# Performance work log

Hardware: AMD Instinct MI355X
Metric: run time of the kernel (lower is better)

## Reference

```python
import jax, jax.numpy as jnp
import numpy as np

B, S, H, HKV, D, BS = 2, 2048, 32, 8, 128, 16
HIDDEN = H * D            # 4096
G = H // HKV              # 4 query heads per kv head
NB = S // BS              # 128 blocks per sequence
SCALE = D ** -0.5


def setup_inputs() -> dict:
    key = jax.random.key(0)
    k1, k2, k3 = jax.random.split(key, 3)
    T = B * S
    hidden_states = jax.random.normal(k1, (T, HIDDEN), dtype=jnp.float32)
    w_qkv = jax.random.normal(k2, (HIDDEN, HIDDEN + 2 * HKV * D), dtype=jnp.float32) * 0.02
    w_out = jax.random.normal(k3, (HIDDEN, HIDDEN), dtype=jnp.float32) * 0.02
    k_cache = jnp.zeros((B * NB, HKV, BS, D), dtype=jnp.float32)
    v_cache = jnp.zeros((B * NB, HKV, BS, D), dtype=jnp.float32)
    block_tables = jnp.arange(B * NB, dtype=jnp.int32).reshape(B, NB)
    return {"hidden_states": hidden_states, "w_qkv": w_qkv, "w_out": w_out,
            "k_cache": k_cache, "v_cache": v_cache, "block_tables": block_tables}


def reference(hidden_states, w_qkv, w_out, k_cache, v_cache, block_tables):
    # qkv projection on packed tokens [T, hidden]
    qkv = hidden_states @ w_qkv
    q, k, v = jnp.split(qkv, [HIDDEN, HIDDEN + HKV * D], axis=-1)
    q = q.reshape(B, S, H, D)
    k = k.reshape(B, S, HKV, D)
    v = v.reshape(B, S, HKV, D)

    # --- paged KV store: scatter per-block pages into cache via block_tables ---
    # [B, NB, BS, HKV, D] -> page layout [B, NB, HKV, BS, D]
    k_pages = k.reshape(B, NB, BS, HKV, D).transpose(0, 1, 3, 2, 4)
    v_pages = v.reshape(B, NB, BS, HKV, D).transpose(0, 1, 3, 2, 4)
    k_cache = k_cache.at[block_tables].set(k_pages)
    v_cache = v_cache.at[block_tables].set(v_pages)

    # --- paged KV gather for prefill attention ---
    kg = k_cache[block_tables].transpose(0, 2, 1, 3, 4).reshape(B, HKV, S, D)
    vg = v_cache[block_tables].transpose(0, 2, 1, 3, 4).reshape(B, HKV, S, D)

    # GQA causal attention: group query heads per kv head
    qh = q.transpose(0, 2, 1, 3).reshape(B, HKV, G, S, D)
    scores = jnp.einsum('bhgqd,bhkd->bhgqk', qh, kg) * SCALE
    causal = jnp.tril(jnp.ones((S, S), dtype=bool))
    scores = jnp.where(causal, scores, -jnp.inf)
    attn = jax.nn.softmax(scores, axis=-1)
    out = jnp.einsum('bhgqk,bhkd->bhgqd', attn, vg)   # [B,HKV,G,S,D]
    out = out.reshape(B, H, S, D).transpose(0, 2, 1, 3).reshape(B * S, HIDDEN)
    return out @ w_out
```

## Files before the change

kernel.cpp:

```cpp
#include <hip/hip_runtime.h>

#define BB 2
#define SS 2048
#define HH 32
#define HKV 8
#define DD 128
#define HIDDEN 4096
#define NQK 6144
#define TT 4096
#define SCALE 0.08838834764831843f
#define SCALE_LOG2E 0.12751743444f

typedef __attribute__((ext_vector_type(8), __may_alias__)) short short8;
typedef __attribute__((ext_vector_type(4), __may_alias__)) short short4v;
typedef __attribute__((ext_vector_type(4), __may_alias__)) float floatx4;

__device__ __forceinline__ short f2bf(float x) {
    unsigned u = __builtin_bit_cast(unsigned, x);
    u += 0x7FFFu + ((u >> 16) & 1u);
    return (short)(u >> 16);
}

__device__ __forceinline__ void gload_lds16(const short* g, short* l) {
    __builtin_amdgcn_global_load_lds((const __attribute__((address_space(1))) void*)g,
                                     (__attribute__((address_space(3))) void*)l, 16, 0, 0);
}

__global__ __launch_bounds__(256) void cvt_f32_bf16(const float* __restrict__ src,
                                                    short* __restrict__ dst) {
    int i = blockIdx.x * 256 + threadIdx.x;
    typedef __attribute__((ext_vector_type(4), __may_alias__)) float f4;
    f4 v = ((const f4*)src)[i];
    short4v o = { f2bf(v.x), f2bf(v.y), f2bf(v.z), f2bf(v.w) };
    ((short4v*)dst)[i] = o;
}

__global__ __launch_bounds__(256) void transpose_cvt(const float* __restrict__ src,
                                                     short* __restrict__ dst,
                                                     int rows, int cols) {
    __shared__ float t[32][33];
    int tx = threadIdx.x, ty = threadIdx.y;
    int c0 = blockIdx.x * 32, r0 = blockIdx.y * 32;
#pragma unroll
    for (int i = 0; i < 32; i += 8) t[ty + i][tx] = src[(size_t)(r0 + ty + i) * cols + c0 + tx];
    __syncthreads();
#pragma unroll
    for (int i = 0; i < 32; i += 8)
        dst[(size_t)(c0 + ty + i) * rows + r0 + tx] = f2bf(t[tx][ty + i]);
}

__global__ __launch_bounds__(256) void build_vt(const short* __restrict__ qkv,
                                                short* __restrict__ vt) {
    __shared__ short t[32][33];
    int tx = threadIdx.x, ty = threadIdx.y;
    int s0 = blockIdx.x * 32, d0 = blockIdx.y * 32;
    int bh = blockIdx.z; int b = bh >> 3, hk = bh & 7;
#pragma unroll
    for (int i = 0; i < 32; i += 8)
        t[ty + i][tx] = qkv[(size_t)(b * SS + s0 + ty + i) * NQK + 5120 + hk * DD + d0 + tx];
    __syncthreads();
#pragma unroll
    for (int i = 0; i < 32; i += 8)
        vt[(size_t)(bh * DD + d0 + ty + i) * SS + s0 + tx] = t[tx][ty + i];
}

template <int OUT_BF16>
__global__ __launch_bounds__(512, 2) void gemm_bt(const short* __restrict__ A,
                                                  const short* __restrict__ Bt,
                                                  void* __restrict__ Cout,
                                                  int M, int N, int K) {
    (void)M;
    __shared__ __align__(16) short smem[65536];
    const int tid  = threadIdx.x;
    const int wave = tid >> 6, lane = tid & 63;
    const int qn = lane & 15, quad = lane >> 4;
    const int wm = wave >> 2, wn = wave & 3;

    int nwg = gridDim.x * gridDim.y;
    int bid = blockIdx.y * gridDim.x + blockIdx.x;
    int q8 = nwg >> 3, r8 = nwg & 7, xcd = bid & 7, boff = bid >> 3;
    int swz = (xcd < r8 ? xcd * (q8 + 1) : r8 * (q8 + 1) + (xcd - r8) * q8) + boff;
    const int n0 = (swz % gridDim.x) * 256;
    const int m0 = (swz / gridDim.x) * 256;

    const int NT = K >> 6;

    const int srow = tid >> 3;
    const int scg  = (tid & 7) ^ (srow & 7);
    const short* aS = A  + (size_t)(m0 + srow) * K + scg * 8;
    const short* bS = Bt + (size_t)(n0 + srow) * K + scg * 8;
    const int lwo = wave * 512;

#define STAGE_A(buf, blk, tt) gload_lds16(aS + (size_t)(blk) * 64 * K + (size_t)(tt) * 64, \
                                          smem + (buf) + (blk) * 4096 + lwo)
#define STAGE_B(buf, blk, tt) gload_lds16(bS + (size_t)(blk) * 64 * K + (size_t)(tt) * 64, \
                                          smem + (buf) + 16384 + (blk) * 4096 + lwo)

    const int xorm  = (qn & 7) << 3;
    const int a_row = (wm * 128 + qn) * 64;
    const int b_row = (wn * 64 + qn) * 64;
    const int col0  = (quad * 8) ^ xorm;
    const int col1  = col0 ^ 32;

#pragma unroll
    for (int blk = 0; blk < 4; blk++) { STAGE_A(0, blk, 0); STAGE_B(0, blk, 0); }
    if (NT > 1) {
#pragma unroll
        for (int blk = 0; blk < 4; blk++) { STAGE_A(32768, blk, 1); STAGE_B(32768, blk, 1); }
        asm volatile("s_waitcnt vmcnt(8)" ::: "memory");
    } else {
        asm volatile("s_waitcnt vmcnt(0)" ::: "memory");
    }
    __builtin_amdgcn_s_barrier();

    floatx4 acc[8][4] = {};

#pragma unroll 2
    for (int t = 0; t < NT; ++t) {
        const int cb = (t & 1) << 15;
        const short* Ab = smem + cb;
        const short* Bb = smem + cb + 16384;
        short8 a[4][2], b0[2][2], b1[2][2], a2[4][2];

#pragma unroll
        for (int mt = 0; mt < 4; mt++) {
            a[mt][0] = *(const short8*)(Ab + a_row + mt * 1024 + col0);
            a[mt][1] = *(const short8*)(Ab + a_row + mt * 1024 + col1);
        }
#pragma unroll
        for (int nt = 0; nt < 2; nt++) {
            b0[nt][0] = *(const short8*)(Bb + b_row + nt * 1024 + col0);
            b0[nt][1] = *(const short8*)(Bb + b_row + nt * 1024 + col1);
        }
        asm volatile("s_waitcnt lgkmcnt(8)" ::: "memory");
        __builtin_amdgcn_s_barrier();
        asm volatile("s_waitcnt lgkmcnt(0)" ::: "memory");
        __builtin_amdgcn_s_setprio(1);
#pragma unroll
        for (int mt = 0; mt < 4; mt++)
#pragma unroll
            for (int nt = 0; nt < 2; nt++) {
                acc[mt][nt] = __builtin_amdgcn_mfma_f32_16x16x32_bf16(a[mt][0], b0[nt][0], acc[mt][nt], 0, 0, 0);
                acc[mt][nt] = __builtin_amdgcn_mfma_f32_16x16x32_bf16(a[mt][1], b0[nt][1], acc[mt][nt], 0, 0, 0);
            }
        __builtin_amdgcn_s_setprio(0);
        __builtin_amdgcn_s_barrier();

#pragma unroll
        for (int nt = 0; nt < 2; nt++) {
            b1[nt][0] = *(const short8*)(Bb + b_row + 2048 + nt * 1024 + col0);
            b1[nt][1] = *(const short8*)(Bb + b_row + 2048 + nt * 1024 + col1);
        }
        if (t + 2 < NT) { STAGE_A(cb, 0, t + 2); STAGE_A(cb, 2, t + 2); }
        __builtin_amdgcn_s_barrier();
        asm volatile("s_waitcnt lgkmcnt(0)" ::: "memory");
        __builtin_amdgcn_s_setprio(1);
#pragma unroll
        for (int mt = 0; mt < 4; mt++)
#pragma unroll
            for (int nt = 0; nt < 2; nt++) {
                acc[mt][2 + nt] = __builtin_amdgcn_mfma_f32_16x16x32_bf16(a[mt][0], b1[nt][0], acc[mt][2 + nt], 0, 0, 0);
                acc[mt][2 + nt] = __builtin_amdgcn_mfma_f32_16x16x32_bf16(a[mt][1], b1[nt][1], acc[mt][2 + nt], 0, 0, 0);
            }
        __builtin_amdgcn_s_setprio(0);
        __builtin_amdgcn_s_barrier();

#pragma unroll
        for (int mt = 0; mt < 4; mt++) {
            a2[mt][0] = *(const short8*)(Ab + 4096 + a_row + mt * 1024 + col0);
            a2[mt][1] = *(const short8*)(Ab + 4096 + a_row + mt * 1024 + col1);
        }
        if (t + 2 < NT) { STAGE_B(cb, 0, t + 2); STAGE_B(cb, 1, t + 2);
                          STAGE_B(cb, 2, t + 2); STAGE_B(cb, 3, t + 2); }
        __builtin_amdgcn_s_barrier();
        asm volatile("s_waitcnt lgkmcnt(0)" ::: "memory");
        __builtin_amdgcn_s_setprio(1);
#pragma unroll
        for (int mt = 0; mt < 4; mt++)
#pragma unroll
            for (int nt = 0; nt < 2; nt++) {
                acc[4 + mt][2 + nt] = __builtin_amdgcn_mfma_f32_16x16x32_bf16(a2[mt][0], b1[nt][0], acc[4 + mt][2 + nt], 0, 0, 0);
                acc[4 + mt][2 + nt] = __builtin_amdgcn_mfma_f32_16x16x32_bf16(a2[mt][1], b1[nt][1], acc[4 + mt][2 + nt], 0, 0, 0);
            }
        __builtin_amdgcn_s_setprio(0);
        __builtin_amdgcn_s_barrier();

        if (t + 2 < NT) { STAGE_A(cb, 1, t + 2); STAGE_A(cb, 3, t + 2); }
        __builtin_amdgcn_s_setprio(1);
#pragma unroll
        for (int mt = 0; mt < 4; mt++)
#pragma unroll
            for (int nt = 0; nt < 2; nt++) {
                acc[4 + mt][nt] = __builtin_amdgcn_mfma_f32_16x16x32_bf16(a2[mt][0], b0[nt][0], acc[4 + mt][nt], 0, 0, 0);
                acc[4 + mt][nt] = __builtin_amdgcn_mfma_f32_16x16x32_bf16(a2[mt][1], b0[nt][1], acc[4 + mt][nt], 0, 0, 0);
            }
        __builtin_amdgcn_s_setprio(0);
        if (t + 2 < NT) asm volatile("s_waitcnt vmcnt(8)" ::: "memory");
        else            asm volatile("s_waitcnt vmcnt(0)" ::: "memory");
        __builtin_amdgcn_s_barrier();
    }
#undef STAGE_A
#undef STAGE_B

    const int erow = m0 + wm * 128 + quad * 4;
    const int ecol = n0 + wn * 64 + qn;
#pragma unroll
    for (int mt = 0; mt < 8; mt++)
#pragma unroll
        for (int nt = 0; nt < 4; nt++)
#pragma unroll
            for (int r = 0; r < 4; r++) {
                size_t off = (size_t)(erow + mt * 16 + r) * N + ecol + nt * 16;
                if (OUT_BF16) ((short*)Cout)[off] = f2bf(acc[mt][nt][r]);
                else          ((float*)Cout)[off] = acc[mt][nt][r];
            }
}

__global__ __launch_bounds__(256) void attn_kernel(const short* __restrict__ qkv,
                                                   const short* __restrict__ vt,
                                                   short* __restrict__ out) {
    __shared__ __align__(16) short Ks[32 * 136];
    __shared__ __align__(16) short Vs[128 * 40];
    __shared__ __align__(16) short Ps[4 * 32 * 40];
    int tid = threadIdx.x, wave = tid >> 6, lane = tid & 63;
    int qn = lane & 15, quad = lane >> 4;
    int bid = blockIdx.x;
    int qt = 63 - (bid >> 4);
    int b  = (bid >> 3) & 1;
    int hk = bid & 7;
    int qb = qt * 32;
    int h  = hk * 4 + wave;
    int bh = b * 8 + hk;

    short8 qf[2][4];
#pragma unroll
    for (int nt = 0; nt < 2; nt++) {
        const short* qrow = qkv + (size_t)(b * SS + qb + nt * 16 + qn) * NQK + h * DD;
#pragma unroll
        for (int c = 0; c < 4; c++) qf[nt][c] = *(const short8*)(qrow + c * 32 + quad * 8);
    }
    const short8 onesv = { 0x3F80, 0x3F80, 0x3F80, 0x3F80, 0x3F80, 0x3F80, 0x3F80, 0x3F80 };
    floatx4 oacc[8][2] = {};
    floatx4 lacc[2] = {};
    int ntiles = qt + 1;

    for (int it = 0; it < ntiles; ++it) {
        int kb = it * 32;
        __syncthreads();
#pragma unroll
        for (int z = 0; z < 2; z++) {
            int ci = z * 256 + tid;
            int key = ci >> 4, dc = ci & 15;
            *(short8*)(Ks + key * 136 + dc * 8) =
                *(const short8*)(qkv + (size_t)(b * SS + kb + key) * NQK + HIDDEN + hk * DD + dc * 8);
        }
#pragma unroll
        for (int z = 0; z < 2; z++) {
            int ci = z * 256 + tid;
            int d = ci >> 2, kc = ci & 3;
            *(short8*)(Vs + d * 40 + kc * 8) =
                *(const short8*)(vt + (size_t)(bh * DD + d) * SS + kb + kc * 8);
        }
        __syncthreads();

        floatx4 sc[2][2] = {};
#pragma unroll
        for (int c = 0; c < 4; c++) {
            short8 k0 = *(const short8*)(Ks + qn * 136 + c * 32 + quad * 8);
            short8 k1 = *(const short8*)(Ks + (16 + qn) * 136 + c * 32 + quad * 8);
#pragma unroll
            for (int nt = 0; nt < 2; nt++) {
                sc[0][nt] = __builtin_amdgcn_mfma_f32_16x16x32_bf16(k0, qf[nt][c], sc[0][nt], 0, 0, 0);
                sc[1][nt] = __builtin_amdgcn_mfma_f32_16x16x32_bf16(k1, qf[nt][c], sc[1][nt], 0, 0, 0);
            }
        }
        bool lastt = (it == ntiles - 1);
        float p[2][8];
#pragma unroll
        for (int nt = 0; nt < 2; nt++)
#pragma unroll
            for (int kt = 0; kt < 2; kt++)
#pragma unroll
                for (int r = 0; r < 4; r++) {
                    float e = exp2f(sc[kt][nt][r] * SCALE_LOG2E);
                    bool masked = lastt && (kb + kt * 16 + quad * 4 + r > qb + nt * 16 + qn);
                    p[nt][kt * 4 + r] = masked ? 0.f : e;
                }

        short* pw = Ps + wave * (32 * 40);
#pragma unroll
        for (int nt = 0; nt < 2; nt++)
#pragma unroll
            for (int kt = 0; kt < 2; kt++) {
                short4v pk = { f2bf(p[nt][kt * 4 + 0]), f2bf(p[nt][kt * 4 + 1]),
                               f2bf(p[nt][kt * 4 + 2]), f2bf(p[nt][kt * 4 + 3]) };
                *(short4v*)(pw + (nt * 16 + qn) * 40 + kt * 16 + quad * 4) = pk;
            }
        short8 pf[2];
#pragma unroll
        for (int nt = 0; nt < 2; nt++)
            pf[nt] = *(const short8*)(pw + (nt * 16 + qn) * 40 + quad * 8);
#pragma unroll
        for (int dt = 0; dt < 8; dt++) {
            short8 vf = *(const short8*)(Vs + (dt * 16 + qn) * 40 + quad * 8);
#pragma unroll
            for (int nt = 0; nt < 2; nt++)
                oacc[dt][nt] = __builtin_amdgcn_mfma_f32_16x16x32_bf16(vf, pf[nt], oacc[dt][nt], 0, 0, 0);
        }
#pragma unroll
        for (int nt = 0; nt < 2; nt++)
            lacc[nt] = __builtin_amdgcn_mfma_f32_16x16x32_bf16(onesv, pf[nt], lacc[nt], 0, 0, 0);
    }
#pragma unroll
    for (int nt = 0; nt < 2; nt++) {
        float inv = 1.0f / lacc[nt][0];
        short* orow = out + (size_t)(b * SS + qb + nt * 16 + qn) * HIDDEN + h * DD;
#pragma unroll
        for (int dt = 0; dt < 8; dt++) {
            short4v ov = { f2bf(oacc[dt][nt][0] * inv), f2bf(oacc[dt][nt][1] * inv),
                           f2bf(oacc[dt][nt][2] * inv), f2bf(oacc[dt][nt][3] * inv) };
            *(short4v*)(orow + dt * 16 + quad * 4) = ov;
        }
    }
}

extern "C" void kernel_launch(void* const* d_in, const int* in_sizes, int n_in,
                              void* d_out, int out_size, void* d_ws, size_t ws_size,
                              hipStream_t stream) {
    (void)in_sizes; (void)n_in; (void)out_size; (void)ws_size;
    const float* hs    = (const float*)d_in[0];
    const float* w_qkv = (const float*)d_in[1];
    const float* w_out = (const float*)d_in[2];

    char* ws = (char*)d_ws;
    short* hsb   = (short*)(ws);
    short* wqkvT = (short*)(ws + 33554432);
    short* woutT = (short*)(ws + 83886080);
    short* qkv   = (short*)(ws + 117440512);
    short* vtb   = (short*)(ws + 167772160);
    short* attnb = (short*)(ws + 176160768);

    cvt_f32_bf16<<<16384, 256, 0, stream>>>(hs, hsb);
    transpose_cvt<<<dim3(192, 128), dim3(32, 8), 0, stream>>>(w_qkv, wqkvT, HIDDEN, NQK);
    transpose_cvt<<<dim3(128, 128), dim3(32, 8), 0, stream>>>(w_out, woutT, HIDDEN, HIDDEN);
    gemm_bt<1><<<dim3(NQK / 256, TT / 256), 512, 0, stream>>>(hsb, wqkvT, qkv, TT, NQK, HIDDEN);
    build_vt<<<dim3(64, 4, 16), dim3(32, 8), 0, stream>>>(qkv, vtb);
    attn_kernel<<<1024, 256, 0, stream>>>(qkv, vtb, attnb);
    gemm_bt<0><<<dim3(HIDDEN / 256, TT / 256), 512, 0, stream>>>(attnb, woutT, d_out, TT, HIDDEN, HIDDEN);
}
```

Measured before the change: 735.1 us.

## Prefetch next K/V tile into registers and remap GEMM workgroups per XCD

The attention loop now loads the next K and V tile from global memory into registers while the current tile is computed, then stores them to LDS at the start of the next iteration. The barrier moves to the end of the iteration, so global-load latency can overlap with MFMA and softmax work. The GEMM workgroup-to-tile mapping is also replaced with a fixed 2x4 XCD tiling that keeps each XCD on a contiguous block of M and N tiles for better L2 reuse. The new mapping hardcodes 16 M-tiles and assumes grid dimensions divisible by the layout, and the prefetch raises register pressure.

```diff
diff --git a/kernel.cpp b/kernel.cpp
--- a/kernel.cpp
+++ b/kernel.cpp
@@ -76,12 +76,13 @@
     const int qn = lane & 15, quad = lane >> 4;
     const int wm = wave >> 2, wn = wave & 3;
 
-    int nwg = gridDim.x * gridDim.y;
     int bid = blockIdx.y * gridDim.x + blockIdx.x;
-    int q8 = nwg >> 3, r8 = nwg & 7, xcd = bid & 7, boff = bid >> 3;
-    int swz = (xcd < r8 ? xcd * (q8 + 1) : r8 * (q8 + 1) + (xcd - r8) * q8) + boff;
-    const int n0 = (swz % gridDim.x) * 256;
-    const int m0 = (swz / gridDim.x) * 256;
+    int xcd = bid & 7, idx = bid >> 3;
+    int bnx = gridDim.x >> 2;
+    int xm = xcd & 1, xn = xcd >> 1;
+    int im = idx & 7, in_ = idx >> 3;
+    const int m0 = (xm * 8 + im) * 256;
+    const int n0 = (xn * bnx + in_) * 256;
 
     const int NT = K >> 6;
 
@@ -244,24 +245,38 @@
     floatx4 lacc[2] = {};
     int ntiles = qt + 1;
 
+    const int kKey0 = tid >> 4,        kDc = tid & 15;
+    const int vD0   = tid >> 2,        vKc = tid & 3;
+    const short* kSrc = qkv + (size_t)(b * SS) * NQK + HIDDEN + hk * DD + kDc * 8;
+    const short* vSrc = vt + (size_t)(bh * DD) * SS + vKc * 8;
+
+    short8 kr[2], vr[2];
+#pragma unroll
+    for (int z = 0; z < 2; z++)
+        kr[z] = *(const short8*)(kSrc + (size_t)(kKey0 + z * 16) * NQK);
+#pragma unroll
+    for (int z = 0; z < 2; z++)
+        vr[z] = *(const short8*)(vSrc + (size_t)(vD0 + z * 64) * SS);
+
     for (int it = 0; it < ntiles; ++it) {
         int kb = it * 32;
+#pragma unroll
+        for (int z = 0; z < 2; z++)
+            *(short8*)(Ks + (kKey0 + z * 16) * 136 + kDc * 8) = kr[z];
+#pragma unroll
+        for (int z = 0; z < 2; z++)
+            *(short8*)(Vs + (vD0 + z * 64) * 40 + vKc * 8) = vr[z];
         __syncthreads();
-#pragma unroll
-        for (int z = 0; z < 2; z++) {
-            int ci = z * 256 + tid;
-            int key = ci >> 4, dc = ci & 15;
-            *(short8*)(Ks + key * 136 + dc * 8) =
-                *(const short8*)(qkv + (size_t)(b * SS + kb + key) * NQK + HIDDEN + hk * DD + dc * 8);
-        }
-#pragma unroll
-        for (int z = 0; z < 2; z++) {
-            int ci = z * 256 + tid;
-            int d = ci >> 2, kc = ci & 3;
-            *(short8*)(Vs + d * 40 + kc * 8) =
-                *(const short8*)(vt + (size_t)(bh * DD + d) * SS + kb + kc * 8);
-        }
-        __syncthreads();
+
+        if (it + 1 < ntiles) {
+            int kb2 = kb + 32;
+#pragma unroll
+            for (int z = 0; z < 2; z++)
+                kr[z] = *(const short8*)(kSrc + (size_t)(kb2 + kKey0 + z * 16) * NQK);
+#pragma unroll
+            for (int z = 0; z < 2; z++)
+                vr[z] = *(const short8*)(vSrc + kb2 + (size_t)(vD0 + z * 64) * SS);
+        }
 
         floatx4 sc[2][2] = {};
 #pragma unroll
@@ -310,6 +325,7 @@
 #pragma unroll
         for (int nt = 0; nt < 2; nt++)
             lacc[nt] = __builtin_amdgcn_mfma_f32_16x16x32_bf16(onesv, pf[nt], lacc[nt], 0, 0, 0);
+        __syncthreads();
     }
 #pragma unroll
     for (int nt = 0; nt < 2; nt++) {
```

After: 720.8 us. Within noise of the previous version (-1.9%).

## Double-buffer attention K/V tiles via async LDS loads and remap GEMM tile-to-XCD

Applied to the files above, without the earlier changes.

The attention kernel now stages 64-key K and V tiles into double-buffered LDS with direct global-to-LDS loads and an XOR swizzle, prefetching the next tile while computing the current one. This halves the barriers per key and hides global load latency. MFMA phases get raised wave priority. The GEMM block-to-XCD mapping also changes so each XCD owns a 2D patch of tiles, aiming at better L2 reuse; the hardcoded mapping assumes particular grid sizes.

```diff
diff --git a/kernel.cpp b/kernel.cpp
--- a/kernel.cpp
+++ b/kernel.cpp
@@ -76,12 +76,13 @@
     const int qn = lane & 15, quad = lane >> 4;
     const int wm = wave >> 2, wn = wave & 3;
 
-    int nwg = gridDim.x * gridDim.y;
     int bid = blockIdx.y * gridDim.x + blockIdx.x;
-    int q8 = nwg >> 3, r8 = nwg & 7, xcd = bid & 7, boff = bid >> 3;
-    int swz = (xcd < r8 ? xcd * (q8 + 1) : r8 * (q8 + 1) + (xcd - r8) * q8) + boff;
-    const int n0 = (swz % gridDim.x) * 256;
-    const int m0 = (swz / gridDim.x) * 256;
+    int xcd = bid & 7, idx = bid >> 3;
+    int bnx = gridDim.x >> 2;
+    int xm = xcd & 1, xn = xcd >> 1;
+    int im = idx & 7, in_ = idx >> 3;
+    const int m0 = (xm * 8 + im) * 256;
+    const int n0 = (xn * bnx + in_) * 256;
 
     const int NT = K >> 6;
 
@@ -219,8 +220,8 @@
 __global__ __launch_bounds__(256) void attn_kernel(const short* __restrict__ qkv,
                                                    const short* __restrict__ vt,
                                                    short* __restrict__ out) {
-    __shared__ __align__(16) short Ks[32 * 136];
-    __shared__ __align__(16) short Vs[128 * 40];
+    __shared__ __align__(16) short Kb[2 * 64 * 128];
+    __shared__ __align__(16) short Vb[2 * 128 * 64];
     __shared__ __align__(16) short Ps[4 * 32 * 40];
     int tid = threadIdx.x, wave = tid >> 6, lane = tid & 63;
     int qn = lane & 15, quad = lane >> 4;
@@ -242,75 +243,95 @@
     const short8 onesv = { 0x3F80, 0x3F80, 0x3F80, 0x3F80, 0x3F80, 0x3F80, 0x3F80, 0x3F80 };
     floatx4 oacc[8][2] = {};
     floatx4 lacc[2] = {};
-    int ntiles = qt + 1;
-
-    for (int it = 0; it < ntiles; ++it) {
-        int kb = it * 32;
+    const int nmac = (qt + 2) >> 1;
+
+    const int kRow = tid >> 4;
+    const int kCgp = (tid & 15) ^ (kRow & 7);
+    const int vRow = tid >> 3;
+    const int vCgp = (tid & 7) ^ (vRow & 7);
+    const short* kSrc = qkv + (size_t)(b * SS) * NQK + HIDDEN + hk * DD + kCgp * 8;
+    const short* vSrc = vt + (size_t)(bh * DD) * SS + vCgp * 8;
+    short* kDst = Kb + wave * 512;
+    short* vDst = Vb + wave * 512;
+
+#define STAGEKV(buf, kb) do {                                                          \
+    _Pragma("unroll")                                                                  \
+    for (int c = 0; c < 4; c++)                                                        \
+        gload_lds16(kSrc + (size_t)((kb) + c * 16 + kRow) * NQK,                       \
+                    kDst + (buf) * 8192 + c * 2048);                                   \
+    _Pragma("unroll")                                                                  \
+    for (int c = 0; c < 4; c++)                                                        \
+        gload_lds16(vSrc + (size_t)(c * 32 + vRow) * SS + (kb),                        \
+                    vDst + (buf) * 8192 + c * 2048);                                   \
+    } while (0)
+
+    STAGEKV(0, 0);
+    __syncthreads();
+
+    const int kxor = (qn & 7) * 8;
+
+    for (int it = 0; it < nmac; ++it) {
+        const int cur = it & 1;
+        if (it + 1 < nmac) STAGEKV(cur ^ 1, (it + 1) * 64);
+        const short* Kc = Kb + cur * 8192;
+        const short* Vc = Vb + cur * 8192;
+
+#pragma unroll
+        for (int s = 0; s < 2; ++s) {
+            const int kb_s = it * 64 + s * 32;
+            if (kb_s > qb) break;
+            const bool needMask = (kb_s == qb);
+
+            floatx4 sc[2][2] = {};
+#pragma unroll
+            for (int c = 0; c < 4; c++) {
+                int cg = ((c * 4 + quad) * 8) ^ kxor;
+                short8 k0 = *(const short8*)(Kc + (s * 32 + qn) * 128 + cg);
+                short8 k1 = *(const short8*)(Kc + (s * 32 + 16 + qn) * 128 + cg);
+#pragma unroll
+                for (int nt = 0; nt < 2; nt++) {
+                    sc[0][nt] = __builtin_amdgcn_mfma_f32_16x16x32_bf16(k0, qf[nt][c], sc[0][nt], 0, 0, 0);
+                    sc[1][nt] = __builtin_amdgcn_mfma_f32_16x16x32_bf16(k1, qf[nt][c], sc[1][nt], 0, 0, 0);
+                }
+            }
+
+            short* pw = Ps + wave * (32 * 40);
+#pragma unroll
+            for (int nt = 0; nt < 2; nt++)
+#pragma unroll
+                for (int kt = 0; kt < 2; kt++) {
+                    float e[4];
+#pragma unroll
+                    for (int r = 0; r < 4; r++) {
+                        float v = exp2f(sc[kt][nt][r] * SCALE_LOG2E);
+                        bool masked = needMask && (kb_s + kt * 16 + quad * 4 + r > qb + nt * 16 + qn);
+                        e[r] = masked ? 0.f : v;
+                    }
+                    short4v pk = { f2bf(e[0]), f2bf(e[1]), f2bf(e[2]), f2bf(e[3]) };
+                    *(short4v*)(pw + (nt * 16 + qn) * 40 + kt * 16 + quad * 4) = pk;
+                }
+            short8 pf[2];
+#pragma unroll
+            for (int nt = 0; nt < 2; nt++)
+                pf[nt] = *(const short8*)(pw + (nt * 16 + qn) * 40 + quad * 8);
+
+            __builtin_amdgcn_s_setprio(1);
+#pragma unroll
+            for (int dt = 0; dt < 8; dt++) {
+                short8 vf = *(const short8*)(Vc + (dt * 16 + qn) * 64 + ((((s << 2) + quad) * 8) ^ kxor));
+#pragma unroll
+                for (int nt = 0; nt < 2; nt++)
+                    oacc[dt][nt] = __builtin_amdgcn_mfma_f32_16x16x32_bf16(vf, pf[nt], oacc[dt][nt], 0, 0, 0);
+            }
+#pragma unroll
+            for (int nt = 0; nt < 2; nt++)
+                lacc[nt] = __builtin_amdgcn_mfma_f32_16x16x32_bf16(onesv, pf[nt], lacc[nt], 0, 0, 0);
+            __builtin_amdgcn_s_setprio(0);
+        }
         __syncthreads();
-#pragma unroll
-        for (int z = 0; z < 2; z++) {
-            int ci = z * 256 + tid;
-            int key = ci >> 4, dc = ci & 15;
-            *(short8*)(Ks + key * 136 + dc * 8) =
-                *(const short8*)(qkv + (size_t)(b * SS + kb + key) * NQK + HIDDEN + hk * DD + dc * 8);
-        }
-#pragma unroll
-        for (int z = 0; z < 2; z++) {
-            int ci = z * 256 + tid;
-            int d = ci >> 2, kc = ci & 3;
-            *(short8*)(Vs + d * 40 + kc * 8) =
-                *(const short8*)(vt + (size_t)(bh * DD + d) * SS + kb + kc * 8);
-        }
-        __syncthreads();
-
-        floatx4 sc[2][2] = {};
-#pragma unroll
-        for (int c = 0; c < 4; c++) {
-            short8 k0 = *(const short8*)(Ks + qn * 136 + c * 32 + quad * 8);
-            short8 k1 = *(const short8*)(Ks + (16 + qn) * 136 + c * 32 + quad * 8);
-#pragma unroll
-            for (int nt = 0; nt < 2; nt++) {
-                sc[0][nt] = __builtin_amdgcn_mfma_f32_16x16x32_bf16(k0, qf[nt][c], sc[0][nt], 0, 0, 0);
-                sc[1][nt] = __builtin_amdgcn_mfma_f32_16x16x32_bf16(k1, qf[nt][c], sc[1][nt], 0, 0, 0);
-            }
-        }
-        bool lastt = (it == ntiles - 1);
-        float p[2][8];
-#pragma unroll
-        for (int nt = 0; nt < 2; nt++)
-#pragma unroll
-            for (int kt = 0; kt < 2; kt++)
-#pragma unroll
-                for (int r = 0; r < 4; r++) {
-                    float e = exp2f(sc[kt][nt][r] * SCALE_LOG2E);
-                    bool masked = lastt && (kb + kt * 16 + quad * 4 + r > qb + nt * 16 + qn);
-                    p[nt][kt * 4 + r] = masked ? 0.f : e;
-                }
-
-        short* pw = Ps + wave * (32 * 40);
-#pragma unroll
-        for (int nt = 0; nt < 2; nt++)
-#pragma unroll
-            for (int kt = 0; kt < 2; kt++) {
-                short4v pk = { f2bf(p[nt][kt * 4 + 0]), f2bf(p[nt][kt * 4 + 1]),
-                               f2bf(p[nt][kt * 4 + 2]), f2bf(p[nt][kt * 4 + 3]) };
-                *(short4v*)(pw + (nt * 16 + qn) * 40 + kt * 16 + quad * 4) = pk;
-            }
-        short8 pf[2];
-#pragma unroll
-        for (int nt = 0; nt < 2; nt++)
-            pf[nt] = *(const short8*)(pw + (nt * 16 + qn) * 40 + quad * 8);
-#pragma unroll
-        for (int dt = 0; dt < 8; dt++) {
-            short8 vf = *(const short8*)(Vs + (dt * 16 + qn) * 40 + quad * 8);
-#pragma unroll
-            for (int nt = 0; nt < 2; nt++)
-                oacc[dt][nt] = __builtin_amdgcn_mfma_f32_16x16x32_bf16(vf, pf[nt], oacc[dt][nt], 0, 0, 0);
-        }
-#pragma unroll
-        for (int nt = 0; nt < 2; nt++)
-            lacc[nt] = __builtin_amdgcn_mfma_f32_16x16x32_bf16(onesv, pf[nt], lacc[nt], 0, 0, 0);
-    }
+    }
+#undef STAGEKV
+
 #pragma unroll
     for (int nt = 0; nt < 2; nt++) {
         float inv = 1.0f / lacc[nt][0];
```

After: 734.7 us. About the same (-0.1%).
